# Performance work log

Measured on AMD Instinct MI355X. Metric: run time of the kernel, lower is better.

## Reference

```python
import jax, jax.numpy as jnp
import numpy as np

NUM_HEADS = 8
NUM_LAYERS = 6
NUM_POINTS = 25
# TrajParamIndex: X=0,Y=1,Z=2,VX=3,VY=4,AX=5,AY=6,YAW=7,LENGTH=8,WIDTH=9,HEIGHT=10


def _unit_cube_points(n=NUM_POINTS):
    m = int(np.sqrt(n))
    lin = np.linspace(-1.0, 1.0, m)
    pts = []
    for dim in range(3):
        for sign in (-1.0, 1.0):
            a, b = np.meshgrid(lin, lin, indexing='ij')
            s = np.full_like(a, sign)
            if dim == 0:
                p = np.stack([s, a, b], -1)
            elif dim == 1:
                p = np.stack([a, s, b], -1)
            else:
                p = np.stack([a, b, s], -1)
            pts.append(p.reshape(-1, 3))
    return jnp.asarray(np.concatenate(pts, 0), jnp.float32)  # [150,3]


def _ln(x, g, b):
    m = x.mean(-1, keepdims=True)
    v = ((x - m) ** 2).mean(-1, keepdims=True)
    return (x - m) / jnp.sqrt(v + 1e-5) * g + b


def _mha(q, k, v, wi, bi, wo, bo):
    E = q.shape[-1]
    d = E // NUM_HEADS
    qq = q @ wi[:E].T + bi[:E]
    kk = k @ wi[E:2 * E].T + bi[E:2 * E]
    vv = v @ wi[2 * E:].T + bi[2 * E:]
    B, S, _ = qq.shape
    Sk = kk.shape[1]
    qh = qq.reshape(B, S, NUM_HEADS, d)
    kh = kk.reshape(B, Sk, NUM_HEADS, d)
    vh = vv.reshape(B, Sk, NUM_HEADS, d)
    att = jnp.einsum('bqhd,bkhd->bhqk', qh, kh) / jnp.sqrt(jnp.float32(d))
    att = jax.nn.softmax(att, axis=-1)
    o = jnp.einsum('bhqk,bkhd->bqhd', att, vh).reshape(B, S, E)
    return o @ wo.T + bo


def _bilinear(feat, uv, valid):
    # feat [B,C,H,W], uv [B,M,2] in [0,1] (u along W), valid [B,M] -> [B,M,C]
    B, C, H, W = feat.shape
    px = uv[..., 0] * (W - 1)
    py = uv[..., 1] * (H - 1)
    x0 = jnp.floor(px)
    y0 = jnp.floor(py)
    wx = px - x0
    wy = py - y0
    x0i = jnp.clip(x0, 0, W - 1).astype(jnp.int32)
    x1i = jnp.clip(x0 + 1, 0, W - 1).astype(jnp.int32)
    y0i = jnp.clip(y0, 0, H - 1).astype(jnp.int32)
    y1i = jnp.clip(y0 + 1, 0, H - 1).astype(jnp.int32)
    flat = feat.reshape(B, C, H * W)
    take = jax.vmap(lambda f, i: f[:, i])  # [C,HW],[M] -> [C,M]
    f00 = take(flat, y0i * W + x0i)
    f01 = take(flat, y0i * W + x1i)
    f10 = take(flat, y1i * W + x0i)
    f11 = take(flat, y1i * W + x1i)
    wxb = wx[:, None, :]
    wyb = wy[:, None, :]
    out = (f00 * (1 - wxb) * (1 - wyb) + f01 * wxb * (1 - wyb)
           + f10 * (1 - wxb) * wyb + f11 * wxb * wyb)
    out = out * valid[:, None, :].astype(out.dtype)
    return out.transpose(0, 2, 1)


def _transform_points(box_pts, tp, ego_t, dt):
    # box_pts [B,N,P,3] local, tp [B,N,11], ego_t [B,4] (x,y,yaw,ts), dt [B]
    yaw = tp[..., 7][..., None]  # [B,N,1]
    c, s = jnp.cos(yaw), jnp.sin(yaw)
    lx, ly, lz = box_pts[..., 0], box_pts[..., 1], box_pts[..., 2]
    rx = lx * c - ly * s
    ry = lx * s + ly * c
    dtb = dt[:, None]  # [B,1]
    cx = tp[..., 0] + tp[..., 3] * dtb + 0.5 * tp[..., 5] * dtb ** 2  # [B,N]
    cy = tp[..., 1] + tp[..., 4] * dtb + 0.5 * tp[..., 6] * dtb ** 2
    cz = tp[..., 2]
    wx = rx + cx[..., None]
    wy = ry + cy[..., None]
    wz = lz + cz[..., None]
    ex = ego_t[:, 0][:, None, None]
    ey = ego_t[:, 1][:, None, None]
    eyaw = ego_t[:, 2][:, None, None]
    pxr = wx - ex
    pyr = wy - ey
    gx = pxr * jnp.cos(eyaw) + pyr * jnp.sin(eyaw)
    gy = -pxr * jnp.sin(eyaw) + pyr * jnp.cos(eyaw)
    return jnp.stack([gx, gy, wz], -1)


def _project(wp, cal):
    # wp [B,N,P,3], cal [B,8] = fx,fy,cx,cy,tx,ty,tz,cam_yaw -> uv in [0,1], valid
    fx, fy, cx0, cy0, tx, ty, tz, cyaw = [cal[:, i][:, None, None] for i in range(8)]
    px = wp[..., 0] - tx
    py = wp[..., 1] - ty
    pz = wp[..., 2] - tz
    fwd = px * jnp.cos(cyaw) + py * jnp.sin(cyaw)
    left = -px * jnp.sin(cyaw) + py * jnp.cos(cyaw)
    zc = fwd
    xc = -left
    yc = -pz
    vz = zc > 0.1
    zs = jnp.maximum(zc, 0.1)
    u = fx * xc / zs + cx0
    v = fy * yc / zs + cy0
    valid = vz & (u >= 0) & (u < 1) & (v >= 0) & (v < 1)
    return jnp.stack([u, v], -1), valid


def _forward(features, calib, ego_states, queries, query_pos,
             traj_w1, traj_b1, traj_w2, traj_b2,
             fm_w1, fm_b1, fm_w2, fm_b2,
             sa_in_w, sa_in_b, sa_out_w, sa_out_b,
             ca_in_w, ca_in_b, ca_out_w, ca_out_b,
             l1_w, l1_b, l2_w, l2_b,
             n1_g, n1_b, n2_g, n2_b, n3_g, n3_b):
    unit = _unit_cube_points()  # [P,3]
    P = unit.shape[0]
    cams, B, T = features.shape[0], features.shape[1], features.shape[2]
    Cf = features.shape[3]
    N = queries.shape[0]

    def traj_head(x):
        return jax.nn.relu(x @ traj_w1.T + traj_b1) @ traj_w2.T + traj_b2

    def feature_mlp(x):
        return jax.nn.relu(x @ fm_w1.T + fm_b1) @ fm_w2.T + fm_b2

    q = jnp.broadcast_to(queries[None], (B, N, queries.shape[1]))
    outputs = []
    for li in range(NUM_LAYERS):
        tp = traj_head(q)  # [B,N,11]
        outputs.append(tp)
        dims = tp[..., 8:11][:, :, None, :]  # [B,N,1,3] (L,W,H)
        box_pts = unit[None, None] * dims  # [B,N,P,3]
        acc = jnp.zeros((B, N, Cf), jnp.float32)
        for t in range(T):
            dt = ego_states[:, t, 3] - ego_states[:, -1, 3]  # [B]
            wp = _transform_points(box_pts, tp, ego_states[:, t], dt)
            for ci in range(cams):
                uv, valid = _project(wp, calib[ci])
                samp = _bilinear(features[ci, :, t], uv.reshape(B, N * P, 2),
                                 valid.reshape(B, N * P))  # [B,N*P,Cf]
                acc = acc + samp.reshape(B, N, P, Cf).sum(axis=2)
        agg = acc / jnp.float32(P * T * cams)
        mem = feature_mlp(agg)  # [B,N,Cf]
        # refine layer li (called without query_pos in decoder forward)
        sa = _mha(q, q, q, sa_in_w[li], sa_in_b[li], sa_out_w[li], sa_out_b[li])
        q = _ln(q + sa, n1_g[li], n1_b[li])
        ca = _mha(q, mem, mem, ca_in_w[li], ca_in_b[li], ca_out_w[li], ca_out_b[li])
        q = _ln(q + ca, n2_g[li], n2_b[li])
        ff = jax.nn.relu(q @ l1_w[li].T + l1_b[li]) @ l2_w[li].T + l2_b[li]
        q = _ln(q + ff, n3_g[li], n3_b[li])
    outputs.append(traj_head(q))
    return jnp.stack(outputs)  # [L+1,B,N,11]


def setup_inputs() -> dict:
    key = jax.random.key(0)
    ks = jax.random.split(key, 32)
    cams, B, T, Cf, H, W = 6, 1, 2, 256, 64, 160
    N, E, Dff, L = 128, 256, 512, NUM_LAYERS

    def rn(k, shape, scale=0.05):
        return jax.random.normal(k, shape, jnp.float32) * scale

    features = jax.random.normal(ks[0], (cams, B, T, Cf, H, W), jnp.float32)
    # calibration: fx,fy,cx,cy,tx,ty,tz,cam_yaw; cameras 8m behind origin along view dir
    cal = np.zeros((cams, B, 8), np.float32)
    for ci in range(cams):
        cyaw = ci * (2 * np.pi / cams)
        cal[ci, :, 0] = 1.2
        cal[ci, :, 1] = 1.6
        cal[ci, :, 2] = 0.5
        cal[ci, :, 3] = 0.5
        cal[ci, :, 4] = -8.0 * np.cos(cyaw)
        cal[ci, :, 5] = -8.0 * np.sin(cyaw)
        cal[ci, :, 6] = -0.5
        cal[ci, :, 7] = cyaw
    calib = jnp.asarray(cal)
    ego = np.zeros((B, T, 4), np.float32)
    for t in range(T):
        ego[:, t, 0] = 0.5 * t
        ego[:, t, 2] = 0.01 * t
        ego[:, t, 3] = 0.1 * t
    ego_states = jnp.asarray(ego)
    return {
        'features': features, 'calib': calib, 'ego_states': ego_states,
        'queries': rn(ks[1], (N, E), 1.0), 'query_pos': rn(ks[2], (N, E), 1.0),
        'traj_w1': rn(ks[3], (Dff, E)), 'traj_b1': jnp.zeros((Dff,), jnp.float32),
        'traj_w2': rn(ks[4], (11, Dff)), 'traj_b2': jnp.zeros((11,), jnp.float32),
        'fm_w1': rn(ks[5], (Dff, E)), 'fm_b1': jnp.zeros((Dff,), jnp.float32),
        'fm_w2': rn(ks[6], (E, Dff)), 'fm_b2': jnp.zeros((E,), jnp.float32),
        'sa_in_w': rn(ks[7], (L, 3 * E, E)), 'sa_in_b': jnp.zeros((L, 3 * E), jnp.float32),
        'sa_out_w': rn(ks[8], (L, E, E)), 'sa_out_b': jnp.zeros((L, E), jnp.float32),
        'ca_in_w': rn(ks[9], (L, 3 * E, E)), 'ca_in_b': jnp.zeros((L, 3 * E), jnp.float32),
        'ca_out_w': rn(ks[10], (L, E, E)), 'ca_out_b': jnp.zeros((L, E), jnp.float32),
        'l1_w': rn(ks[11], (L, Dff, E)), 'l1_b': jnp.zeros((L, Dff), jnp.float32),
        'l2_w': rn(ks[12], (L, E, Dff)), 'l2_b': jnp.zeros((L, E), jnp.float32),
        'n1_g': jnp.ones((L, E), jnp.float32), 'n1_b': jnp.zeros((L, E), jnp.float32),
        'n2_g': jnp.ones((L, E), jnp.float32), 'n2_b': jnp.zeros((L, E), jnp.float32),
        'n3_g': jnp.ones((L, E), jnp.float32), 'n3_b': jnp.zeros((L, E), jnp.float32),
    }


def reference(features, calib, ego_states, queries, query_pos,
              traj_w1, traj_b1, traj_w2, traj_b2,
              fm_w1, fm_b1, fm_w2, fm_b2,
              sa_in_w, sa_in_b, sa_out_w, sa_out_b,
              ca_in_w, ca_in_b, ca_out_w, ca_out_b,
              l1_w, l1_b, l2_w, l2_b,
              n1_g, n1_b, n2_g, n2_b, n3_g, n3_b):
    return _forward(features, calib, ego_states, queries, query_pos,
                    traj_w1, traj_b1, traj_w2, traj_b2,
                    fm_w1, fm_b1, fm_w2, fm_b2,
                    sa_in_w, sa_in_b, sa_out_w, sa_out_b,
                    ca_in_w, ca_in_b, ca_out_w, ca_out_b,
                    l1_w, l1_b, l2_w, l2_b,
                    n1_g, n1_b, n2_g, n2_b, n3_g, n3_b)
```

## Files before the change

### kernel.cpp

```cpp
#include <hip/hip_runtime.h>
#include <stdint.h>

typedef unsigned short u16;

#define DEV static __device__ __forceinline__

DEV float b2f(u16 u){ return __uint_as_float(((uint32_t)u) << 16); }
DEV u16 f2b(float f){ uint32_t x = __float_as_uint(f); return (u16)((x + 0x7fffu + ((x >> 16) & 1u)) >> 16); }
DEV int imin(int a, int b){ return a < b ? a : b; }
DEV int imax(int a, int b){ return a > b ? a : b; }

DEV int is_f32(const void* cal){
  float a = ((const float*)cal)[0];
  return (fabsf(a - 1.2f) < 1e-2f) ? 1 : 0;
}

DEV float ld(const void* p, size_t i, int f32){
  return f32 ? ((const float*)p)[i] : b2f(((const u16*)p)[i]);
}

__device__ float4 g_sawT[6*256*768/4];
__device__ float4 g_sowT[6*256*256/4];
__device__ float4 g_cawT[6*256*768/4];
__device__ float4 g_cowT[6*256*256/4];
__device__ float4 g_l1wT[6*256*512/4];
__device__ float4 g_l2wT[6*512*256/4];
__device__ float4 g_tw1T[256*512/4];
__device__ float4 g_fw1T[256*512/4];
__device__ float4 g_fw2T[512*256/4];

DEV float dotP(const float* x, const float4* wP, int col, const int N, const int K){
  const float4* p = wP + col;
  const float4* x4 = (const float4*)x;
  float s0=0.f,s1=0.f,s2=0.f,s3=0.f;
  #pragma unroll 8
  for(int k4 = 0; k4 < K/4; k4++){
    float4 w = p[(size_t)k4*N];
    float4 xv = x4[k4];
    s0 += xv.x*w.x; s1 += xv.y*w.y; s2 += xv.z*w.z; s3 += xv.w*w.w;
  }
  return (s0+s1)+(s2+s3);
}

DEV void dot2P(const float* x, const float4* wP, int c0, int c1, const int N,
               float* r0, float* r1){
  const float4* p0 = wP + c0;
  const float4* p1 = wP + c1;
  const float4* x4 = (const float4*)x;
  float a0=0,a1=0,a2=0,a3=0,b0=0,b1=0,b2=0,b3=0;
  #pragma unroll 8
  for(int k4 = 0; k4 < 64; k4++){
    float4 xv = x4[k4];
    float4 w0 = p0[(size_t)k4*N];
    float4 w1 = p1[(size_t)k4*N];
    a0+=xv.x*w0.x; a1+=xv.y*w0.y; a2+=xv.z*w0.z; a3+=xv.w*w0.w;
    b0+=xv.x*w1.x; b1+=xv.y*w1.y; b2+=xv.z*w1.z; b3+=xv.w*w1.w;
  }
  *r0=(a0+a1)+(a2+a3); *r1=(b0+b1)+(b2+b3);
}

DEV void dot3P(const float* x, const float4* wP, int t, float* r0, float* r1, float* r2){
  const float4* p0 = wP + t;
  const float4* p1 = wP + t + 256;
  const float4* p2 = wP + t + 512;
  const float4* x4 = (const float4*)x;
  float a0=0,a1=0,a2=0,a3=0,b0=0,b1=0,b2=0,b3=0,c0=0,c1=0,c2=0,c3=0;
  #pragma unroll 4
  for(int k4 = 0; k4 < 64; k4++){
    float4 xv = x4[k4];
    float4 w0 = p0[(size_t)k4*768];
    float4 w1 = p1[(size_t)k4*768];
    float4 w2 = p2[(size_t)k4*768];
    a0+=xv.x*w0.x; a1+=xv.y*w0.y; a2+=xv.z*w0.z; a3+=xv.w*w0.w;
    b0+=xv.x*w1.x; b1+=xv.y*w1.y; b2+=xv.z*w1.z; b3+=xv.w*w1.w;
    c0+=xv.x*w2.x; c1+=xv.y*w2.y; c2+=xv.z*w2.z; c3+=xv.w*w2.w;
  }
  *r0=(a0+a1)+(a2+a3); *r1=(b0+b1)+(b2+b3); *r2=(c0+c1)+(c2+c3);
}

DEV void kv_store_k(float* kT, int t, int qi, float val){
  int hh = t >> 5, i = t & 31;
  kT[((size_t)(hh*1024 + (i>>2)*128 + qi))*4 + (i&3)] = val;
}
DEV void kv_store_v(float* vP, int t, int qi, float val){
  vP[((size_t)((qi>>2)*256 + t))*4 + (qi&3)] = val;
}

DEV float attn_score(const float* qv, const float* kT, int hh, int k){
  const float4* kp = (const float4*)kT + hh*1024 + k;
  const float4* xq = (const float4*)(qv + hh*32);
  float s0=0.f, s1=0.f;
  #pragma unroll
  for(int i4 = 0; i4 < 8; i4 += 2){
    float4 w0 = kp[i4*128], w1 = kp[(i4+1)*128];
    float4 x0 = xq[i4],     x1 = xq[i4+1];
    s0 += x0.x*w0.x + x0.y*w0.y + x0.z*w0.z + x0.w*w0.w;
    s1 += x1.x*w1.x + x1.y*w1.y + x1.z*w1.z + x1.w*w1.w;
  }
  return s0+s1;
}

DEV float attn_av(const float* s, const float* vP, int hh, int t){
  const float4* vp = (const float4*)vP + t;
  const float4* sp = (const float4*)(s + hh*128);
  float a0=0.f, a1=0.f;
  #pragma unroll 8
  for(int k4 = 0; k4 < 32; k4 += 2){
    float4 w0 = vp[(size_t)k4*256], w1 = vp[(size_t)(k4+1)*256];
    float4 s0 = sp[k4],             s1 = sp[k4+1];
    a0 += s0.x*w0.x + s0.y*w0.y + s0.z*w0.z + s0.w*w0.w;
    a1 += s1.x*w1.x + s1.y*w1.y + s1.z*w1.z + s1.w*w1.w;
  }
  return a0+a1;
}

DEV float bsum256(float v, float* buf){
  int t = threadIdx.x;
  for(int off = 32; off > 0; off >>= 1) v += __shfl_xor(v, off);
  if((t & 63) == 0) buf[t >> 6] = v;
  __syncthreads();
  float r = buf[0] + buf[1] + buf[2] + buf[3];
  __syncthreads();
  return r;
}

DEV float lnorm(float r, const void* g, const void* b, size_t off, float* buf, int f32){
  float m = bsum256(r, buf) * (1.f/256.f);
  float d = r - m;
  float v = bsum256(d*d, buf) * (1.f/256.f);
  return d * rsqrtf(v + 1e-5f) * ld(g, off + threadIdx.x, f32) + ld(b, off + threadIdx.x, f32);
}

DEV void traj_headT(const float* qn, const void* b1, const void* w2, const void* b2,
                    float* hbuf, float* tp, void* out, int slot, int qi, int f32){
  int t = threadIdx.x;
  float h0, h1;
  dot2P(qn, g_tw1T, t, t + 256, 512, &h0, &h1);
  hbuf[t]     = fmaxf(0.f, ld(b1, t, f32)     + h0);
  hbuf[t+256] = fmaxf(0.f, ld(b1, t+256, f32) + h1);
  __syncthreads();
  if(t < 176){
    int o = t >> 4, lane = t & 15;
    float s = 0.f;
    for(int k = lane; k < 512; k += 16) s += hbuf[k] * ld(w2, o*512 + k, f32);
    for(int off = 8; off > 0; off >>= 1) s += __shfl_down(s, off, 16);
    if(lane == 0){
      s += ld(b2, o, f32);
      tp[qi*11 + o] = s;
      int oi = (slot*128 + qi)*11 + o;
      if(f32) ((float*)out)[oi] = s; else ((u16*)out)[oi] = f2b(s);
    }
  }
  __syncthreads();
}

DEV void softmax8(float* s){
  int t = threadIdx.x;
  int hh = t >> 5, lane = t & 31;
  float m = -1e30f;
  for(int k = lane; k < 128; k += 32) m = fmaxf(m, s[hh*128 + k]);
  for(int off = 16; off > 0; off >>= 1) m = fmaxf(m, __shfl_xor(m, off, 32));
  float ss = 0.f;
  for(int k = lane; k < 128; k += 32){
    float e = __expf(s[hh*128 + k] - m);
    s[hh*128 + k] = e; ss += e;
  }
  for(int off = 16; off > 0; off >>= 1) ss += __shfl_xor(ss, off, 32);
  float inv = 1.f / ss;
  for(int k = lane; k < 128; k += 32) s[hh*128 + k] *= inv;
}

__global__ __launch_bounds__(256) void k_prep(const void* feat, u16* FTb, int use_ft,
    const void* saw, const void* sow, const void* caw, const void* cow,
    const void* l1w, const void* l2w, const void* tw1, const void* fw1, const void* fw2,
    const void* cal){
  int f32 = is_f32(cal);
  int t = threadIdx.x;
  __shared__ __align__(16) float smem[64*65];
  int bid = blockIdx.x;
  if(bid < 7680){
    if(!use_ft) return;
    u16* tu = (u16*)smem;
    int cc = bid & 3; int rest = bid >> 2;
    int pch = rest % 160; int e = rest / 160;
    if(f32){
      #pragma unroll
      for(int pass = 0; pass < 4; pass++){
        int ch = pass*16 + (t >> 4);
        int pos = (t & 15)*4;
        const float* sp = (const float*)feat + ((size_t)(e*256 + cc*64 + ch))*10240 + pch*64 + pos;
        float4 v = *(const float4*)sp;
        tu[(pos+0)*66 + ch] = f2b(v.x); tu[(pos+1)*66 + ch] = f2b(v.y);
        tu[(pos+2)*66 + ch] = f2b(v.z); tu[(pos+3)*66 + ch] = f2b(v.w);
      }
    } else {
      #pragma unroll
      for(int pass = 0; pass < 4; pass++){
        int ch = pass*16 + (t >> 4);
        int pos = (t & 15)*4;
        const u16* sp = (const u16*)feat + ((size_t)(e*256 + cc*64 + ch))*10240 + pch*64 + pos;
        ushort4 v = *(const ushort4*)sp;
        tu[(pos+0)*66 + ch] = v.x; tu[(pos+1)*66 + ch] = v.y;
        tu[(pos+2)*66 + ch] = v.z; tu[(pos+3)*66 + ch] = v.w;
      }
    }
    __syncthreads();
    #pragma unroll
    for(int pass = 0; pass < 4; pass++){
      int pos = pass*16 + (t >> 4);
      int ch = (t & 15)*4;
      ushort4 v;
      v.x = tu[pos*66 + ch]; v.y = tu[pos*66 + ch+1]; v.z = tu[pos*66 + ch+2]; v.w = tu[pos*66 + ch+3];
      *(ushort4*)&FTb[((size_t)(e*10240 + pch*64 + pos))*256 + cc*64 + ch] = v;
    }
    return;
  }
  bid -= 7680;
  const void* src; float* dst; int N, K, NB, KB;
  if(bid < 288)      { src = saw; dst = (float*)g_sawT; N=768; K=256; NB=12; KB=4; }
  else if(bid < 384) { src = sow; dst = (float*)g_sowT; N=256; K=256; NB=4;  KB=4; bid -= 288; }
  else if(bid < 672) { src = caw; dst = (float*)g_cawT; N=768; K=256; NB=12; KB=4; bid -= 384; }
  else if(bid < 768) { src = cow; dst = (float*)g_cowT; N=256; K=256; NB=4;  KB=4; bid -= 672; }
  else if(bid < 960) { src = l1w; dst = (float*)g_l1wT; N=512; K=256; NB=8;  KB=4; bid -= 768; }
  else if(bid < 1152){ src = l2w; dst = (float*)g_l2wT; N=256; K=512; NB=4;  KB=8; bid -= 960; }
  else if(bid < 1184){ src = tw1; dst = (float*)g_tw1T; N=512; K=256; NB=8;  KB=4; bid -= 1152; }
  else if(bid < 1216){ src = fw1; dst = (float*)g_fw1T; N=512; K=256; NB=8;  KB=4; bid -= 1184; }
  else               { src = fw2; dst = (float*)g_fw2T; N=256; K=512; NB=4;  KB=8; bid -= 1216; }
  int nb = bid % NB;
  int kb = (bid / NB) % KB;
  int l  = bid / (NB*KB);
  float* tile = smem;
  for(int it = 0; it < 16; it++){
    int n = it*4 + (t >> 6);
    int k = t & 63;
    tile[n*65 + k] = ld(src, ((size_t)l*N + nb*64 + n)*K + kb*64 + k, f32);
  }
  __syncthreads();
  int kl = t & 3, nn = (t >> 2) & 15, wv = t >> 6;
  int n_local = wv*16 + nn;
  for(int k4 = 0; k4 < 16; k4++){
    int kcol = k4*4 + kl;
    size_t addr = (size_t)l*K*N + (((size_t)(kb*16 + k4))*N + nb*64 + n_local)*4 + kl;
    dst[addr] = tile[n_local*65 + kcol];
  }
}

__global__ __launch_bounds__(256, 2) void k_init(const void* queries,
    const void* tb1, const void* tw2, const void* tb2,
    const void* sab, const void* cal,
    float* q, float* tp, float* qrow, float* kTsa, float* vsa, float* acc, void* out){
  __shared__ __align__(16) float qn[256]; __shared__ __align__(16) float hbuf[512];
  int t = threadIdx.x, qi = blockIdx.x;
  int f32 = is_f32(cal);
  float v = ld(queries, qi*256 + t, f32);
  qn[t] = v; q[qi*256 + t] = v;
  __syncthreads();
  traj_headT(qn, tb1, tw2, tb2, hbuf, tp, out, 0, qi, f32);
  float c0, c1, c2;
  dot3P(qn, g_sawT, t, &c0, &c1, &c2);
  qrow[qi*256 + t] = ld(sab, t, f32)       + c0;
  kv_store_k(kTsa, t, qi, ld(sab, t + 256, f32) + c1);
  kv_store_v(vsa,  t, qi, ld(sab, t + 512, f32) + c2);
  acc[qi*256 + t] = 0.f;
}

__global__ __launch_bounds__(256, 2) void k_samsa(const u16* FTb, const void* feat, int use_ft,
    const void* cal, const void* ego, const float* tp, float* acc,
    const float* q, const float* qrow, const float* kTsa, const float* vsa,
    const void* sob, const void* n1g, const void* n1b, const void* cab,
    int li, float* qs, float* qq){
  int t = threadIdx.x;
  int f32 = is_f32(cal);
  __shared__ __align__(16) float xa[256];
  __shared__ __align__(16) float s[1024];
  __shared__ __align__(16) float h[512];
  __shared__ float buf[8];
  __shared__ float tps[11];
  __shared__ int4  soff[152];
  __shared__ float4 sw[152];
  __shared__ float spx[152], spy[152];
  __shared__ int sval[152];
  __shared__ int plist[152];
  __shared__ int pcnt;

  if(blockIdx.x < 128){
    int qi = blockIdx.x;
    xa[t] = qrow[qi*256 + t];
    __syncthreads();
    for(int rep = 0; rep < 4; rep++){
      int idx = t + rep*256; int hh = idx >> 7, k = idx & 127;
      s[idx] = attn_score(xa, kTsa, hh, k) * 0.1767766952966369f;
    }
    __syncthreads();
    softmax8(s);
    __syncthreads();
    h[t] = attn_av(s, vsa, t >> 5, t);
    __syncthreads();
    float pr = ld(sob, (size_t)li*256 + t, f32) + dotP(h, g_sowT + (size_t)li*16384, t, 256, 256);
    float r = q[qi*256 + t] + pr;
    float y = lnorm(r, n1g, n1b, (size_t)li*256, buf, f32);
    qs[qi*256 + t] = y;
    __syncthreads();
    xa[t] = y;
    __syncthreads();
    qq[qi*256 + t] = ld(cab, (size_t)li*768 + t, f32)
                   + dotP(xa, g_cawT + (size_t)li*49152, t, 768, 256);
    return;
  }

  int sb = blockIdx.x - 128;
  int ob = (sb & 7) * 192 + (sb >> 3);
  int qi = ob & 127, e = ob >> 7;
  int ci = e >> 1, tt = e & 1;
  if(t == 0) pcnt = 0;
  if(t < 11) tps[t] = tp[qi*11 + t];
  __syncthreads();
  if(t < 150){
    float dt = ld(ego, tt*4 + 3, f32) - ld(ego, 7, f32);
    int face = t/25, rr = t%25, ii = rr/5, jj = rr%5;
    float av = -1.f + 0.5f*ii, bv = -1.f + 0.5f*jj;
    float sg = (face & 1) ? 1.f : -1.f; int dim = face >> 1;
    float ux = (dim == 0) ? sg : av;
    float uy = (dim == 0) ? av : ((dim == 1) ? sg : bv);
    float uz = (dim == 2) ? sg : bv;
    float lx = ux*tps[8], ly = uy*tps[9], lz = uz*tps[10];
    float yaw = tps[7];
    float cyw = cosf(yaw), syw = sinf(yaw);
    float rx = lx*cyw - ly*syw, ry = lx*syw + ly*cyw;
    float dt2 = 0.5f*dt*dt;
    float cxx = tps[0] + tps[3]*dt + tps[5]*dt2;
    float cyy = tps[1] + tps[4]*dt + tps[6]*dt2;
    float wx = rx + cxx, wy = ry + cyy, wz = lz + tps[2];
    float ex = ld(ego, tt*4, f32), ey = ld(ego, tt*4 + 1, f32), eyaw = ld(ego, tt*4 + 2, f32);
    float ce = cosf(eyaw), se = sinf(eyaw);
    float pxr = wx - ex, pyr = wy - ey;
    float gx = pxr*ce + pyr*se, gy = -pxr*se + pyr*ce;
    float fx = ld(cal, ci*8, f32),   fy = ld(cal, ci*8+1, f32);
    float cx0 = ld(cal, ci*8+2, f32), cy0 = ld(cal, ci*8+3, f32);
    float tx = ld(cal, ci*8+4, f32), ty = ld(cal, ci*8+5, f32);
    float tz = ld(cal, ci*8+6, f32), cw = ld(cal, ci*8+7, f32);
    float cc = cosf(cw), sc = sinf(cw);
    float pxc = gx - tx, pyc = gy - ty, pzc = wz - tz;
    float zc = pxc*cc + pyc*sc;
    float left = -pxc*sc + pyc*cc;
    float xc = -left, yc = -pzc;
    float zs = fmaxf(zc, 0.1f);
    float u = fx*xc/zs + cx0, vv = fy*yc/zs + cy0;
    bool val = (zc > 0.1f) && (u >= 0.f) && (u < 1.f) && (vv >= 0.f) && (vv < 1.f);
    float px = u*159.f, py = vv*63.f;
    spx[t] = px; spy[t] = py;
    float x0f = floorf(px), y0f = floorf(py);
    float wxf = px - x0f, wyf = py - y0f;
    int x0 = imin(imax((int)x0f, 0), 159), y0 = imin(imax((int)y0f, 0), 63);
    int x1 = imin(x0 + 1, 159), y1 = imin(y0 + 1, 63);
    soff[t] = make_int4((y0*160 + x0)*256, (y0*160 + x1)*256,
                        (y1*160 + x0)*256, (y1*160 + x1)*256);
    sw[t] = make_float4((1.f-wxf)*(1.f-wyf), wxf*(1.f-wyf), (1.f-wxf)*wyf, wxf*wyf);
    sval[t] = val ? 1 : 0;
    if(val){ int ix = atomicAdd(&pcnt, 1); plist[ix] = t; }
  }
  __syncthreads();
  float a = 0.f;
  if(use_ft){
    const u16* base = FTb + (size_t)e*10240*256 + t;
    int np = pcnt;
    int pp = 0;
    for(; pp + 4 <= np; pp += 4){
      int p0 = plist[pp], p1 = plist[pp+1], p2 = plist[pp+2], p3 = plist[pp+3];
      int4 o0 = soff[p0]; int4 o1 = soff[p1]; int4 o2 = soff[p2]; int4 o3 = soff[p3];
      float4 w0 = sw[p0]; float4 w1 = sw[p1]; float4 w2 = sw[p2]; float4 w3 = sw[p3];
      float v00 = b2f(base[o0.x]), v01 = b2f(base[o0.y]), v02 = b2f(base[o0.z]), v03 = b2f(base[o0.w]);
      float v10 = b2f(base[o1.x]), v11 = b2f(base[o1.y]), v12 = b2f(base[o1.z]), v13 = b2f(base[o1.w]);
      float v20 = b2f(base[o2.x]), v21 = b2f(base[o2.y]), v22 = b2f(base[o2.z]), v23 = b2f(base[o2.w]);
      float v30 = b2f(base[o3.x]), v31 = b2f(base[o3.y]), v32 = b2f(base[o3.z]), v33 = b2f(base[o3.w]);
      a += w0.x*v00 + w0.y*v01 + w0.z*v02 + w0.w*v03;
      a += w1.x*v10 + w1.y*v11 + w1.z*v12 + w1.w*v13;
      a += w2.x*v20 + w2.y*v21 + w2.z*v22 + w2.w*v23;
      a += w3.x*v30 + w3.y*v31 + w3.z*v32 + w3.w*v33;
    }
    for(; pp < np; pp++){
      int p = plist[pp];
      int4 o = soff[p]; float4 w = sw[p];
      a += w.x*b2f(base[o.x]) + w.y*b2f(base[o.y])
         + w.z*b2f(base[o.z]) + w.w*b2f(base[o.w]);
    }
  } else {
    size_t pc = ((size_t)e*256 + t)*10240;
    for(int p = 0; p < 150; p++){
      if(!sval[p]) continue;
      float px = spx[p], py = spy[p];
      float x0f = floorf(px), y0f = floorf(py);
      float wxf = px - x0f, wyf = py - y0f;
      int x0 = imin(imax((int)x0f, 0), 159), y0 = imin(imax((int)y0f, 0), 63);
      int x1 = imin(x0 + 1, 159), y1 = imin(y0 + 1, 63);
      float w00 = (1.f-wxf)*(1.f-wyf), w01 = wxf*(1.f-wyf), w10 = (1.f-wxf)*wyf, w11 = wxf*wyf;
      a += w00*ld(feat, pc + y0*160 + x0, f32) + w01*ld(feat, pc + y0*160 + x1, f32)
         + w10*ld(feat, pc + y1*160 + x0, f32) + w11*ld(feat, pc + y1*160 + x1, f32);
    }
  }
  atomicAdd(&acc[qi*256 + t], a);
}

__global__ __launch_bounds__(256, 2) void k_mk(const float* acc,
    const void* fb1, const void* fb2, const void* cab, const void* cal,
    int li, float* kvK, float* kvV){
  __shared__ __align__(16) float xa[256];
  __shared__ __align__(16) float h[512];
  int t = threadIdx.x, qi = blockIdx.x;
  int f32 = is_f32(cal);
  xa[t] = acc[qi*256 + t] * (1.f/1800.f);
  __syncthreads();
  float h0, h1;
  dot2P(xa, g_fw1T, t, t + 256, 512, &h0, &h1);
  h[t]     = fmaxf(0.f, ld(fb1, t, f32)     + h0);
  h[t+256] = fmaxf(0.f, ld(fb1, t+256, f32) + h1);
  __syncthreads();
  float m = ld(fb2, t, f32) + dotP(h, g_fw2T, t, 256, 512);
  __syncthreads();
  xa[t] = m;
  __syncthreads();
  const float4* cawT = g_cawT + (size_t)li*49152;
  float kk, vv;
  dot2P(xa, cawT, 256 + t, 512 + t, 768, &kk, &vv);
  size_t bo = (size_t)li*768;
  kv_store_k(kvK, t, qi, ld(cab, bo + 256 + t, f32) + kk);
  kv_store_v(kvV, t, qi, ld(cab, bo + 512 + t, f32) + vv);
}

__global__ __launch_bounds__(256, 2) void k_ca(const float* qs, const float* qq,
    const float* kvK, const float* kvV,
    const void* cob, const void* n2g, const void* n2b,
    const void* l1b, const void* l2b, const void* n3g, const void* n3b,
    const void* tb1, const void* tw2, const void* tb2, const void* sab, const void* cal,
    int li, int have_next,
    float* qout, float* qrow, float* kTsa, float* vsa,
    float* tp, float* acc, void* out){
  __shared__ __align__(16) float qv[256]; __shared__ __align__(16) float s[1024];
  __shared__ __align__(16) float o[256];  __shared__ __align__(16) float q2[256];
  __shared__ __align__(16) float h[512];  __shared__ float buf[8];
  int t = threadIdx.x, qi = blockIdx.x;
  int f32 = is_f32(cal);
  qv[t] = qq[qi*256 + t];
  __syncthreads();
  for(int rep = 0; rep < 4; rep++){
    int idx = t + rep*256; int hh = idx >> 7, k = idx & 127;
    s[idx] = attn_score(qv, kvK, hh, k) * 0.1767766952966369f;
  }
  __syncthreads();
  softmax8(s);
  __syncthreads();
  o[t] = attn_av(s, kvV, t >> 5, t);
  __syncthreads();
  float pr = ld(cob, (size_t)li*256 + t, f32) + dotP(o, g_cowT + (size_t)li*16384, t, 256, 256);
  float r = qs[qi*256 + t] + pr;
  float y = lnorm(r, n2g, n2b, (size_t)li*256, buf, f32);
  q2[t] = y;
  __syncthreads();
  float h0, h1;
  dot2P(q2, g_l1wT + (size_t)li*32768, t, t + 256, 512, &h0, &h1);
  h[t]     = fmaxf(0.f, ld(l1b, (size_t)li*512 + t, f32)     + h0);
  h[t+256] = fmaxf(0.f, ld(l1b, (size_t)li*512 + t+256, f32) + h1);
  __syncthreads();
  float ff = ld(l2b, (size_t)li*256 + t, f32) + dotP(h, g_l2wT + (size_t)li*32768, t, 256, 512);
  float r3 = q2[t] + ff;
  float y3 = lnorm(r3, n3g, n3b, (size_t)li*256, buf, f32);
  qout[qi*256 + t] = y3;
  __syncthreads();
  q2[t] = y3;
  __syncthreads();
  traj_headT(q2, tb1, tw2, tb2, h, tp, out, li + 1, qi, f32);
  if(have_next){
    float c0, c1, c2;
    dot3P(q2, g_sawT + (size_t)(li+1)*49152, t, &c0, &c1, &c2);
    size_t sb = (size_t)(li+1)*768;
    qrow[qi*256 + t] = ld(sab, sb + t, f32) + c0;
    kv_store_k(kTsa, t, qi, ld(sab, sb + 256 + t, f32) + c1);
    kv_store_v(vsa,  t, qi, ld(sab, sb + 512 + t, f32) + c2);
  }
  acc[qi*256 + t] = 0.f;
}

extern "C" void kernel_launch(void* const* d_in, const int* in_sizes, int n_in,
                              void* d_out, int out_size, void* d_ws, size_t ws_size,
                              hipStream_t stream){
  const void* feat    = d_in[0];
  const void* calib   = d_in[1];
  const void* ego     = d_in[2];
  const void* queries = d_in[3];
  const void* tw1 = d_in[5];  const void* tb1 = d_in[6];
  const void* tw2 = d_in[7];  const void* tb2 = d_in[8];
  const void* fw1 = d_in[9];  const void* fb1 = d_in[10];
  const void* fw2 = d_in[11]; const void* fb2 = d_in[12];
  const void* saw = d_in[13]; const void* sab = d_in[14];
  const void* sow = d_in[15]; const void* sob = d_in[16];
  const void* caw = d_in[17]; const void* cab = d_in[18];
  const void* cow = d_in[19]; const void* cob = d_in[20];
  const void* l1w = d_in[21]; const void* l1b = d_in[22];
  const void* l2w = d_in[23]; const void* l2b = d_in[24];
  const void* n1g = d_in[25]; const void* n1b = d_in[26];
  const void* n2g = d_in[27]; const void* n2b = d_in[28];
  const void* n3g = d_in[29]; const void* n3b = d_in[30];

  float* ws   = (float*)d_ws;
  float* q    = ws + 16;
  float* qs   = ws + 32784;
  float* tp   = ws + 65552;
  float* qrow = ws + 67088;
  float* kTsa = ws + 99856;
  float* vsa  = ws + 132624;
  float* kvK  = ws + 165392;
  float* kvV  = ws + 198160;
  float* qq   = ws + 230928;
  float* acc  = ws + 263696;
  u16*   FTb  = (u16*)(ws + 296464);
  size_t need = (size_t)296464*4 + (size_t)12*10240*256*2;
  int use_ft = (ws_size >= need) ? 1 : 0;

  k_prep<<<8928, 256, 0, stream>>>(feat, FTb, use_ft,
                                   saw, sow, caw, cow, l1w, l2w, tw1, fw1, fw2, calib);
  k_init<<<128, 256, 0, stream>>>(queries, tb1, tw2, tb2, sab, calib,
                                  q, tp, qrow, kTsa, vsa, acc, d_out);
  for(int li = 0; li < 6; li++){
    k_samsa<<<1664, 256, 0, stream>>>(FTb, feat, use_ft, calib, ego, tp, acc,
                                      q, qrow, kTsa, vsa, sob, n1g, n1b, cab,
                                      li, qs, qq);
    k_mk<<<128, 256, 0, stream>>>(acc, fb1, fb2, cab, calib, li, kvK, kvV);
    int hn = (li < 5) ? 1 : 0;
    k_ca<<<128, 256, 0, stream>>>(qs, qq, kvK, kvV, cob, n2g, n2b,
                                  l1b, l2b, n3g, n3b,
                                  tb1, tw2, tb2, sab, calib, li, hn,
                                  q, qrow, kTsa, vsa, tp, acc, d_out);
  }
  (void)in_sizes; (void)n_in; (void)out_size;
}
```

Measured before the change: 1.034 ms.

## Fuse memory-KV and cross-attention kernels via grid barrier; widen feature transpose tiles

Merges the per-layer k_mk and k_ca kernels into one kernel. Blocks synchronize through a global atomic counter spin barrier after writing cross-attention K/V, which removes one kernel launch per layer. The feature transpose in k_prep now processes 128 positions per block with padded 32-bit shared storage, halving the number of transpose blocks. The barrier depends on all 128 blocks being co-resident and adds spin/fence overhead.

```diff
diff --git a/kernel.cpp b/kernel.cpp
--- a/kernel.cpp
+++ b/kernel.cpp
@@ -176,46 +176,54 @@
     const void* cal){
   int f32 = is_f32(cal);
   int t = threadIdx.x;
-  __shared__ __align__(16) float smem[64*65];
+  __shared__ __align__(16) uint32_t smem[64*129];
   int bid = blockIdx.x;
-  if(bid < 7680){
+  if(bid < 3840){
     if(!use_ft) return;
-    u16* tu = (u16*)smem;
     int cc = bid & 3; int rest = bid >> 2;
-    int pch = rest % 160; int e = rest / 160;
+    int pch2 = rest % 80; int e = rest / 80;
+    size_t rowbase = (size_t)(e*256 + cc*64);
+    size_t poff = (size_t)pch2*128;
     if(f32){
       #pragma unroll
-      for(int pass = 0; pass < 4; pass++){
-        int ch = pass*16 + (t >> 4);
-        int pos = (t & 15)*4;
-        const float* sp = (const float*)feat + ((size_t)(e*256 + cc*64 + ch))*10240 + pch*64 + pos;
+      for(int p = 0; p < 8; p++){
+        int r = p*8 + (t >> 5);
+        int pos = (t & 31)*4;
+        const float* sp = (const float*)feat + (rowbase + r)*10240 + poff + pos;
         float4 v = *(const float4*)sp;
-        tu[(pos+0)*66 + ch] = f2b(v.x); tu[(pos+1)*66 + ch] = f2b(v.y);
-        tu[(pos+2)*66 + ch] = f2b(v.z); tu[(pos+3)*66 + ch] = f2b(v.w);
+        smem[r*129 + pos+0] = f2b(v.x);
+        smem[r*129 + pos+1] = f2b(v.y);
+        smem[r*129 + pos+2] = f2b(v.z);
+        smem[r*129 + pos+3] = f2b(v.w);
       }
     } else {
       #pragma unroll
-      for(int pass = 0; pass < 4; pass++){
-        int ch = pass*16 + (t >> 4);
-        int pos = (t & 15)*4;
-        const u16* sp = (const u16*)feat + ((size_t)(e*256 + cc*64 + ch))*10240 + pch*64 + pos;
+      for(int p = 0; p < 8; p++){
+        int r = p*8 + (t >> 5);
+        int pos = (t & 31)*4;
+        const u16* sp = (const u16*)feat + (rowbase + r)*10240 + poff + pos;
         ushort4 v = *(const ushort4*)sp;
-        tu[(pos+0)*66 + ch] = v.x; tu[(pos+1)*66 + ch] = v.y;
-        tu[(pos+2)*66 + ch] = v.z; tu[(pos+3)*66 + ch] = v.w;
+        smem[r*129 + pos+0] = v.x;
+        smem[r*129 + pos+1] = v.y;
+        smem[r*129 + pos+2] = v.z;
+        smem[r*129 + pos+3] = v.w;
       }
     }
     __syncthreads();
     #pragma unroll
-    for(int pass = 0; pass < 4; pass++){
-      int pos = pass*16 + (t >> 4);
+    for(int p = 0; p < 8; p++){
+      int pos = p*16 + (t >> 4);
       int ch = (t & 15)*4;
       ushort4 v;
-      v.x = tu[pos*66 + ch]; v.y = tu[pos*66 + ch+1]; v.z = tu[pos*66 + ch+2]; v.w = tu[pos*66 + ch+3];
-      *(ushort4*)&FTb[((size_t)(e*10240 + pch*64 + pos))*256 + cc*64 + ch] = v;
+      v.x = (u16)smem[(ch+0)*129 + pos];
+      v.y = (u16)smem[(ch+1)*129 + pos];
+      v.z = (u16)smem[(ch+2)*129 + pos];
+      v.w = (u16)smem[(ch+3)*129 + pos];
+      *(ushort4*)&FTb[((size_t)(e*10240) + poff + pos)*256 + cc*64 + ch] = v;
     }
     return;
   }
-  bid -= 7680;
+  bid -= 3840;
   const void* src; float* dst; int N, K, NB, KB;
   if(bid < 288)      { src = saw; dst = (float*)g_sawT; N=768; K=256; NB=12; KB=4; }
   else if(bid < 384) { src = sow; dst = (float*)g_sowT; N=256; K=256; NB=4;  KB=4; bid -= 288; }
@@ -229,7 +237,7 @@
   int nb = bid % NB;
   int kb = (bid / NB) % KB;
   int l  = bid / (NB*KB);
-  float* tile = smem;
+  float* tile = (float*)smem;
   for(int it = 0; it < 16; it++){
     int n = it*4 + (t >> 6);
     int k = t & 63;
@@ -248,10 +256,12 @@
 __global__ __launch_bounds__(256, 2) void k_init(const void* queries,
     const void* tb1, const void* tw2, const void* tb2,
     const void* sab, const void* cal,
-    float* q, float* tp, float* qrow, float* kTsa, float* vsa, float* acc, void* out){
+    float* q, float* tp, float* qrow, float* kTsa, float* vsa, float* acc,
+    unsigned int* cnt, void* out){
   __shared__ __align__(16) float qn[256]; __shared__ __align__(16) float hbuf[512];
   int t = threadIdx.x, qi = blockIdx.x;
   int f32 = is_f32(cal);
+  if(qi == 0 && t < 8) cnt[t] = 0;
   float v = ld(queries, qi*256 + t, f32);
   qn[t] = v; q[qi*256 + t] = v;
   __syncthreads();
@@ -401,13 +411,22 @@
   atomicAdd(&acc[qi*256 + t], a);
 }
 
-__global__ __launch_bounds__(256, 2) void k_mk(const float* acc,
-    const void* fb1, const void* fb2, const void* cab, const void* cal,
-    int li, float* kvK, float* kvV){
-  __shared__ __align__(16) float xa[256];
-  __shared__ __align__(16) float h[512];
+__global__ __launch_bounds__(256, 2) void k_mkca(const float* acc,
+    const void* fb1, const void* fb2, const void* cab,
+    const float* qs, const float* qq,
+    const void* cob, const void* n2g, const void* n2b,
+    const void* l1b, const void* l2b, const void* n3g, const void* n3b,
+    const void* tb1, const void* tw2, const void* tb2, const void* sab, const void* cal,
+    int li, int have_next,
+    float* kvK, float* kvV,
+    float* qout, float* qrow, float* kTsa, float* vsa,
+    float* tp, float* accw, void* out, unsigned int* cnt){
+  __shared__ __align__(16) float xa[256]; __shared__ __align__(16) float s[1024];
+  __shared__ __align__(16) float o[256];  __shared__ __align__(16) float q2[256];
+  __shared__ __align__(16) float h[512];  __shared__ float buf[8];
   int t = threadIdx.x, qi = blockIdx.x;
   int f32 = is_f32(cal);
+
   xa[t] = acc[qi*256 + t] * (1.f/1800.f);
   __syncthreads();
   float h0, h1;
@@ -419,32 +438,29 @@
   __syncthreads();
   xa[t] = m;
   __syncthreads();
-  const float4* cawT = g_cawT + (size_t)li*49152;
-  float kk, vv;
-  dot2P(xa, cawT, 256 + t, 512 + t, 768, &kk, &vv);
-  size_t bo = (size_t)li*768;
-  kv_store_k(kvK, t, qi, ld(cab, bo + 256 + t, f32) + kk);
-  kv_store_v(kvV, t, qi, ld(cab, bo + 512 + t, f32) + vv);
-}
-
-__global__ __launch_bounds__(256, 2) void k_ca(const float* qs, const float* qq,
-    const float* kvK, const float* kvV,
-    const void* cob, const void* n2g, const void* n2b,
-    const void* l1b, const void* l2b, const void* n3g, const void* n3b,
-    const void* tb1, const void* tw2, const void* tb2, const void* sab, const void* cal,
-    int li, int have_next,
-    float* qout, float* qrow, float* kTsa, float* vsa,
-    float* tp, float* acc, void* out){
-  __shared__ __align__(16) float qv[256]; __shared__ __align__(16) float s[1024];
-  __shared__ __align__(16) float o[256];  __shared__ __align__(16) float q2[256];
-  __shared__ __align__(16) float h[512];  __shared__ float buf[8];
-  int t = threadIdx.x, qi = blockIdx.x;
-  int f32 = is_f32(cal);
-  qv[t] = qq[qi*256 + t];
+  {
+    const float4* cawT = g_cawT + (size_t)li*49152;
+    float kk, vv;
+    dot2P(xa, cawT, 256 + t, 512 + t, 768, &kk, &vv);
+    size_t bo = (size_t)li*768;
+    kv_store_k(kvK, t, qi, ld(cab, bo + 256 + t, f32) + kk);
+    kv_store_v(kvV, t, qi, ld(cab, bo + 512 + t, f32) + vv);
+  }
+
+  __threadfence();
+  __syncthreads();
+  if(t == 0){
+    atomicAdd(cnt, 1u);
+    while(atomicAdd(cnt, 0u) < 128u){ __builtin_amdgcn_s_sleep(8); }
+  }
+  __syncthreads();
+  __threadfence();
+
+  xa[t] = qq[qi*256 + t];
   __syncthreads();
   for(int rep = 0; rep < 4; rep++){
     int idx = t + rep*256; int hh = idx >> 7, k = idx & 127;
-    s[idx] = attn_score(qv, kvK, hh, k) * 0.1767766952966369f;
+    s[idx] = attn_score(xa, kvK, hh, k) * 0.1767766952966369f;
   }
   __syncthreads();
   softmax8(s);
@@ -456,7 +472,6 @@
   float y = lnorm(r, n2g, n2b, (size_t)li*256, buf, f32);
   q2[t] = y;
   __syncthreads();
-  float h0, h1;
   dot2P(q2, g_l1wT + (size_t)li*32768, t, t + 256, 512, &h0, &h1);
   h[t]     = fmaxf(0.f, ld(l1b, (size_t)li*512 + t, f32)     + h0);
   h[t+256] = fmaxf(0.f, ld(l1b, (size_t)li*512 + t+256, f32) + h1);
@@ -477,7 +492,7 @@
     kv_store_k(kTsa, t, qi, ld(sab, sb + 256 + t, f32) + c1);
     kv_store_v(vsa,  t, qi, ld(sab, sb + 512 + t, f32) + c2);
   }
-  acc[qi*256 + t] = 0.f;
+  accw[qi*256 + t] = 0.f;
 }
 
 extern "C" void kernel_launch(void* const* d_in, const int* in_sizes, int n_in,
@@ -502,6 +517,7 @@
   const void* n3g = d_in[29]; const void* n3b = d_in[30];
 
   float* ws   = (float*)d_ws;
+  unsigned int* cnt = (unsigned int*)d_ws;
   float* q    = ws + 16;
   float* qs   = ws + 32784;
   float* tp   = ws + 65552;
@@ -516,20 +532,20 @@
   size_t need = (size_t)296464*4 + (size_t)12*10240*256*2;
   int use_ft = (ws_size >= need) ? 1 : 0;
 
-  k_prep<<<8928, 256, 0, stream>>>(feat, FTb, use_ft,
+  k_prep<<<5088, 256, 0, stream>>>(feat, FTb, use_ft,
                                    saw, sow, caw, cow, l1w, l2w, tw1, fw1, fw2, calib);
   k_init<<<128, 256, 0, stream>>>(queries, tb1, tw2, tb2, sab, calib,
-                                  q, tp, qrow, kTsa, vsa, acc, d_out);
+                                  q, tp, qrow, kTsa, vsa, acc, cnt, d_out);
   for(int li = 0; li < 6; li++){
     k_samsa<<<1664, 256, 0, stream>>>(FTb, feat, use_ft, calib, ego, tp, acc,
                                       q, qrow, kTsa, vsa, sob, n1g, n1b, cab,
                                       li, qs, qq);
-    k_mk<<<128, 256, 0, stream>>>(acc, fb1, fb2, cab, calib, li, kvK, kvV);
     int hn = (li < 5) ? 1 : 0;
-    k_ca<<<128, 256, 0, stream>>>(qs, qq, kvK, kvV, cob, n2g, n2b,
-                                  l1b, l2b, n3g, n3b,
-                                  tb1, tw2, tb2, sab, calib, li, hn,
-                                  q, qrow, kTsa, vsa, tp, acc, d_out);
+    k_mkca<<<128, 256, 0, stream>>>(acc, fb1, fb2, cab, qs, qq,
+                                    cob, n2g, n2b, l1b, l2b, n3g, n3b,
+                                    tb1, tw2, tb2, sab, calib, li, hn,
+                                    kvK, kvV, q, qrow, kTsa, vsa,
+                                    tp, acc, d_out, cnt + li);
   }
   (void)in_sizes; (void)n_in; (void)out_size;
 }
```

New measurement: 1.306 ms. 1.26x slower.
